# Performance work log

Hardware: AMD Instinct MI355X
Metric: run time of the kernel (lower is better)

The kernel has to match this reference:

```python
import jax, jax.numpy as jnp
import numpy as np

N, E, IN, H, D = 20000, 640000, 256, 4, 32
NEG_SLOPE = 0.2


def setup_inputs() -> dict:
    key = jax.random.key(0)
    ks = jax.random.split(key, 8)
    feat = jax.random.normal(ks[0], (N, IN), dtype=jnp.float32)
    pr_score = jax.random.uniform(ks[1], (N,), dtype=jnp.float32) + 1e-3
    edge_src = jax.random.randint(ks[2], (E,), 0, N)
    edge_dst = jax.random.randint(ks[3], (E,), 0, N)
    # parameters (xavier-ish scale)
    fc_w = jax.random.normal(ks[4], (H * D, IN), dtype=jnp.float32) * (2.0 / np.sqrt(IN + H * D))
    attn_l = jax.random.normal(ks[5], (1, H, D), dtype=jnp.float32) * (2.0 / np.sqrt(1 + D))
    attn_r = jax.random.normal(ks[6], (1, H, D), dtype=jnp.float32) * (2.0 / np.sqrt(1 + D))
    bias = jnp.zeros((H * D,), dtype=jnp.float32)
    return {"feat": feat, "pr_score": pr_score, "edge_src": edge_src,
            "edge_dst": edge_dst, "fc_w": fc_w, "attn_l": attn_l,
            "attn_r": attn_r, "bias": bias}


def reference(feat, pr_score, edge_src, edge_dst, fc_w, attn_l, attn_r, bias):
    n = feat.shape[0]
    h, d = attn_l.shape[1], attn_l.shape[2]
    # feat_src = fc(feat).view(N, H, D)
    ft = (feat @ fc_w.T).reshape(n, h, d)                       # [N,H,D]
    el = jnp.sum(ft * attn_l, axis=-1)                          # [N,H]
    er = jnp.sum(ft * attn_r, axis=-1)                          # [N,H]
    e = jax.nn.leaky_relu(el[edge_src] + er[edge_dst], NEG_SLOPE)  # [E,H]
    # edge_softmax over incoming edges per destination node
    emax = jax.ops.segment_max(e, edge_dst, num_segments=n)
    ee = jnp.exp(e - emax[edge_dst])
    esum = jax.ops.segment_sum(ee, edge_dst, num_segments=n)
    a = ee / esum[edge_dst]                                     # [E,H]
    # PageRank-style normalization: b = pr[src] / sum_{in-edges}(pr[src])
    pr_src = pr_score[edge_src]                                 # [E]
    pr_sum = jax.ops.segment_sum(pr_src, edge_dst, num_segments=n)
    b = pr_src / pr_sum[edge_dst]                               # [E]
    c = a * b[:, None]                                          # [E,H]
    csum = jax.ops.segment_sum(c, edge_dst, num_segments=n)
    c = c / csum[edge_dst]                                      # [E,H]
    # weighted aggregation: rst[dst] = sum_e ft[src_e] * c_e
    m = ft[edge_src] * c[:, :, None]                            # [E,H,D]
    rst = jax.ops.segment_sum(m, edge_dst, num_segments=n)      # [N,H,D]
    rst = rst + bias.reshape(1, h, d)
    return rst
```

## Files before the change

kernel.cpp:

```cpp
#include <hip/hip_runtime.h>

#define IN_DIM 256
#define HD 128
#define NHEAD 4
#define NEG_SLOPE 0.2f
#define ELLW 128

typedef unsigned int  uint;
typedef unsigned short ushort_t;

typedef short bf16x8 __attribute__((ext_vector_type(8)));
typedef float f32x4  __attribute__((ext_vector_type(4)));

__device__ __forceinline__ ushort_t f2bf(float x) {
    uint u = __float_as_uint(x);
    u += 0x7fffu + ((u >> 16) & 1u);
    return (ushort_t)(u >> 16);
}
__device__ __forceinline__ uint pack2(float lo, float hi) {
    return (uint)f2bf(lo) | ((uint)f2bf(hi) << 16);
}
__device__ __forceinline__ float bflo(uint u) { return __uint_as_float(u << 16); }
__device__ __forceinline__ float bfhi(uint u) { return __uint_as_float(u & 0xffff0000u); }

#define GBM 64
#define GBK 64
#define LDK 72

__global__ __launch_bounds__(256) void gemm_mfma(
    const float* __restrict__ feat, const float* __restrict__ fcw,
    const float* __restrict__ attn_l, const float* __restrict__ attn_r,
    ushort_t* __restrict__ ft16, float* __restrict__ el, float* __restrict__ er,
    int* __restrict__ deg, int n)
{
    __shared__ ushort_t s_a[GBM * LDK];
    __shared__ ushort_t s_b[128 * LDK];

    const int t    = threadIdx.x;
    {
        const int z = blockIdx.x * 256 + t;
        if (z < n) deg[z] = 0;
    }

    const int row0 = blockIdx.x * GBM;
    const int w    = t >> 6;
    const int lane = t & 63;
    const int fr   = lane & 15;
    const int fq   = lane >> 4;

    f32x4 acc[8];
#pragma unroll
    for (int nt = 0; nt < 8; ++nt) acc[nt] = (f32x4){0.f, 0.f, 0.f, 0.f};

    const int s_row = t >> 2, s_kca = (t & 3) * 16;
    const int s_col = t >> 1, s_kcb = (t & 1) * 32;

    const ushort_t* pa  = &s_a[(w * 16 + fr) * LDK + fq * 8];
    const ushort_t* pb0 = &s_b[fr * LDK + fq * 8];

    for (int k0 = 0; k0 < IN_DIM; k0 += GBK) {
        {
            const int grow = row0 + s_row;
            float4 v0, v1, v2, v3;
            if (grow < n) {
                const float* p = feat + (size_t)grow * IN_DIM + k0 + s_kca;
                v0 = *(const float4*)(p + 0);
                v1 = *(const float4*)(p + 4);
                v2 = *(const float4*)(p + 8);
                v3 = *(const float4*)(p + 12);
            } else {
                v0 = make_float4(0.f,0.f,0.f,0.f); v1 = v0; v2 = v0; v3 = v0;
            }
            uint4* dst = (uint4*)&s_a[s_row * LDK + s_kca];
            dst[0] = make_uint4(pack2(v0.x,v0.y), pack2(v0.z,v0.w),
                                pack2(v1.x,v1.y), pack2(v1.z,v1.w));
            dst[1] = make_uint4(pack2(v2.x,v2.y), pack2(v2.z,v2.w),
                                pack2(v3.x,v3.y), pack2(v3.z,v3.w));
        }
        {
            const float* p = fcw + (size_t)s_col * IN_DIM + k0 + s_kcb;
            uint4* dst = (uint4*)&s_b[s_col * LDK + s_kcb];
#pragma unroll
            for (int q = 0; q < 2; ++q) {
                float4 u0 = *(const float4*)(p + q * 16 + 0);
                float4 u1 = *(const float4*)(p + q * 16 + 4);
                float4 u2 = *(const float4*)(p + q * 16 + 8);
                float4 u3 = *(const float4*)(p + q * 16 + 12);
                dst[2 * q + 0] = make_uint4(pack2(u0.x,u0.y), pack2(u0.z,u0.w),
                                            pack2(u1.x,u1.y), pack2(u1.z,u1.w));
                dst[2 * q + 1] = make_uint4(pack2(u2.x,u2.y), pack2(u2.z,u2.w),
                                            pack2(u3.x,u3.y), pack2(u3.z,u3.w));
            }
        }
        __syncthreads();

        const bf16x8 a0 = *(const bf16x8*)pa;
        const bf16x8 a1 = *(const bf16x8*)(pa + 32);
#pragma unroll
        for (int nt = 0; nt < 8; ++nt) {
            const ushort_t* pb = pb0 + nt * 16 * LDK;
            const bf16x8 b0 = *(const bf16x8*)pb;
            const bf16x8 b1 = *(const bf16x8*)(pb + 32);
            acc[nt] = __builtin_amdgcn_mfma_f32_16x16x32_bf16(a0, b0, acc[nt], 0, 0, 0);
            acc[nt] = __builtin_amdgcn_mfma_f32_16x16x32_bf16(a1, b1, acc[nt], 0, 0, 0);
        }
        __syncthreads();
    }

    float al[8], ar_[8];
#pragma unroll
    for (int nt = 0; nt < 8; ++nt) {
        al[nt]  = attn_l[nt * 16 + fr];
        ar_[nt] = attn_r[nt * 16 + fr];
    }

#pragma unroll
    for (int j = 0; j < 4; ++j) {
        const int grow = row0 + w * 16 + fq * 4 + j;
        const bool ok = grow < n;
        if (ok) {
#pragma unroll
            for (int nt = 0; nt < 8; ++nt)
                ft16[(size_t)grow * HD + nt * 16 + fr] = f2bf(acc[nt][j]);
        }
        float pl0 = acc[0][j]*al[0] + acc[1][j]*al[1];
        float pl1 = acc[2][j]*al[2] + acc[3][j]*al[3];
        float pl2 = acc[4][j]*al[4] + acc[5][j]*al[5];
        float pl3 = acc[6][j]*al[6] + acc[7][j]*al[7];
        float pe0 = acc[0][j]*ar_[0] + acc[1][j]*ar_[1];
        float pe1 = acc[2][j]*ar_[2] + acc[3][j]*ar_[3];
        float pe2 = acc[4][j]*ar_[4] + acc[5][j]*ar_[5];
        float pe3 = acc[6][j]*ar_[6] + acc[7][j]*ar_[7];
#pragma unroll
        for (int m = 1; m < 16; m <<= 1) {
            pl0 += __shfl_xor(pl0, m, 64); pl1 += __shfl_xor(pl1, m, 64);
            pl2 += __shfl_xor(pl2, m, 64); pl3 += __shfl_xor(pl3, m, 64);
            pe0 += __shfl_xor(pe0, m, 64); pe1 += __shfl_xor(pe1, m, 64);
            pe2 += __shfl_xor(pe2, m, 64); pe3 += __shfl_xor(pe3, m, 64);
        }
        if (ok && fr == 0) {
            *(float4*)&el[(size_t)grow * NHEAD] = make_float4(pl0, pl1, pl2, pl3);
            *(float4*)&er[(size_t)grow * NHEAD] = make_float4(pe0, pe1, pe2, pe3);
        }
    }
}

__global__ void build_ell(const int* __restrict__ src, const int* __restrict__ dst,
                          int* __restrict__ deg, int* __restrict__ ell, int e)
{
    int i = blockIdx.x * blockDim.x + threadIdx.x;
    if (i < e) {
        const int d = dst[i];
        const int r = atomicAdd(&deg[d], 1);
        if (r < ELLW) ell[(size_t)d * ELLW + r] = src[i];
    }
}

__global__ __launch_bounds__(256) void aggregate(
    const uint4* __restrict__ ftu4, const float* __restrict__ el,
    const float* __restrict__ er, const float* __restrict__ pr,
    const int* __restrict__ deg, const int* __restrict__ ell,
    const float* __restrict__ bias, float* __restrict__ out, int n)
{
    const int wave = threadIdx.x >> 6;
    const int lane = threadIdx.x & 63;
    const int slot = lane >> 4;
    const int sub  = lane & 15;
    const int head = sub >> 2;
    const int dst  = blockIdx.x * 4 + wave;

    __shared__ float s_w[4][NHEAD][72];
    __shared__ int   s_s[4][72];

    if (dst >= n) return;

    if (lane < 8) {
        s_s[wave][64 + lane] = 0;
#pragma unroll
        for (int hh = 0; hh < NHEAD; ++hh) s_w[wave][hh][64 + lane] = 0.f;
    }

    const int dg  = min(deg[dst], ELLW);
    const int beg = dst * ELLW;
    const float4 e4 = *(const float4*)&er[(size_t)dst * NHEAD];

    float aA[8], aB[8];
#pragma unroll
    for (int i = 0; i < 8; ++i) { aA[i] = 0.f; aB[i] = 0.f; }
    float w0 = 0.f, w1 = 0.f, w2 = 0.f, w3 = 0.f;

    for (int base = 0; base < dg; base += 64) {
        const int len = min(64, dg - base);
        if (lane < len) {
            const int s = ell[beg + base + lane];
            const float p = pr[s];
            const float4 l4 = *(const float4*)&el[(size_t)s * NHEAD];
            float e0 = l4.x + e4.x, e1 = l4.y + e4.y;
            float e2 = l4.z + e4.z, e3 = l4.w + e4.w;
            e0 = e0 > 0.f ? e0 : NEG_SLOPE * e0;
            e1 = e1 > 0.f ? e1 : NEG_SLOPE * e1;
            e2 = e2 > 0.f ? e2 : NEG_SLOPE * e2;
            e3 = e3 > 0.f ? e3 : NEG_SLOPE * e3;
            const float ww0 = __expf(e0) * p;
            const float ww1 = __expf(e1) * p;
            const float ww2 = __expf(e2) * p;
            const float ww3 = __expf(e3) * p;
            s_w[wave][0][lane] = ww0; s_w[wave][1][lane] = ww1;
            s_w[wave][2][lane] = ww2; s_w[wave][3][lane] = ww3;
            s_s[wave][lane] = s;
            w0 += ww0; w1 += ww1; w2 += ww2; w3 += ww3;
        } else {
            s_w[wave][0][lane] = 0.f; s_w[wave][1][lane] = 0.f;
            s_w[wave][2][lane] = 0.f; s_w[wave][3][lane] = 0.f;
            s_s[wave][lane] = 0;
        }
        for (int j = 0; j < len; j += 8) {
            const int eA = j + slot;
            const int eB = j + 4 + slot;
            const int   sA = s_s[wave][eA];
            const int   sB = s_s[wave][eB];
            const float wA = s_w[wave][head][eA];
            const float wB = s_w[wave][head][eB];
            const uint4 uA = ftu4[(size_t)sA * 16 + sub];
            const uint4 uB = ftu4[(size_t)sB * 16 + sub];
            aA[0] = fmaf(wA, bflo(uA.x), aA[0]);
            aA[1] = fmaf(wA, bfhi(uA.x), aA[1]);
            aA[2] = fmaf(wA, bflo(uA.y), aA[2]);
            aA[3] = fmaf(wA, bfhi(uA.y), aA[3]);
            aA[4] = fmaf(wA, bflo(uA.z), aA[4]);
            aA[5] = fmaf(wA, bfhi(uA.z), aA[5]);
            aA[6] = fmaf(wA, bflo(uA.w), aA[6]);
            aA[7] = fmaf(wA, bfhi(uA.w), aA[7]);
            aB[0] = fmaf(wB, bflo(uB.x), aB[0]);
            aB[1] = fmaf(wB, bfhi(uB.x), aB[1]);
            aB[2] = fmaf(wB, bflo(uB.y), aB[2]);
            aB[3] = fmaf(wB, bfhi(uB.y), aB[3]);
            aB[4] = fmaf(wB, bflo(uB.z), aB[4]);
            aB[5] = fmaf(wB, bfhi(uB.z), aB[5]);
            aB[6] = fmaf(wB, bflo(uB.w), aB[6]);
            aB[7] = fmaf(wB, bfhi(uB.w), aB[7]);
        }
    }

    float a[8];
#pragma unroll
    for (int i = 0; i < 8; ++i) a[i] = aA[i] + aB[i];
#pragma unroll
    for (int i = 0; i < 8; ++i) {
        a[i] += __shfl_xor(a[i], 16, 64);
        a[i] += __shfl_xor(a[i], 32, 64);
    }

#pragma unroll
    for (int m = 1; m < 64; m <<= 1) {
        w0 += __shfl_xor(w0, m, 64);
        w1 += __shfl_xor(w1, m, 64);
        w2 += __shfl_xor(w2, m, 64);
        w3 += __shfl_xor(w3, m, 64);
    }

    if (slot == 0) {
        const float denom = (head == 0) ? w0 : (head == 1) ? w1 : (head == 2) ? w2 : w3;
        const float inv = (dg > 0) ? 1.f / denom : 0.f;
        const float4 b0 = *(const float4*)&bias[8 * sub];
        const float4 b1 = *(const float4*)&bias[8 * sub + 4];
        float4 r0, r1;
        r0.x = a[0] * inv + b0.x; r0.y = a[1] * inv + b0.y;
        r0.z = a[2] * inv + b0.z; r0.w = a[3] * inv + b0.w;
        r1.x = a[4] * inv + b1.x; r1.y = a[5] * inv + b1.y;
        r1.z = a[6] * inv + b1.z; r1.w = a[7] * inv + b1.w;
        *(float4*)&out[(size_t)dst * HD + 8 * sub]     = r0;
        *(float4*)&out[(size_t)dst * HD + 8 * sub + 4] = r1;
    }
}

extern "C" void kernel_launch(void* const* d_in, const int* in_sizes, int n_in,
                              void* d_out, int out_size, void* d_ws, size_t ws_size,
                              hipStream_t stream)
{
    const float* feat   = (const float*)d_in[0];
    const float* pr     = (const float*)d_in[1];
    const int*   esrc   = (const int*)d_in[2];
    const int*   edst   = (const int*)d_in[3];
    const float* fcw    = (const float*)d_in[4];
    const float* attn_l = (const float*)d_in[5];
    const float* attn_r = (const float*)d_in[6];
    const float* bias   = (const float*)d_in[7];
    float* out = (float*)d_out;

    const int n = in_sizes[0] / IN_DIM;
    const int e = in_sizes[2];

    char* ws = (char*)d_ws;
    size_t off = 0;
    auto wsalloc = [&](size_t bytes) -> void* {
        void* p = ws + off;
        off += (bytes + 255) & ~(size_t)255;
        return p;
    };
    ushort_t* ft16 = (ushort_t*)wsalloc((size_t)n * HD * sizeof(ushort_t));
    float* el   = (float*)wsalloc((size_t)n * NHEAD * sizeof(float));
    float* er   = (float*)wsalloc((size_t)n * NHEAD * sizeof(float));
    int*   deg  = (int*)wsalloc((size_t)n * sizeof(int));
    int*   ell  = (int*)wsalloc((size_t)n * ELLW * sizeof(int));

    gemm_mfma<<<(n + GBM - 1) / GBM, 256, 0, stream>>>(feat, fcw, attn_l, attn_r,
                                                       ft16, el, er, deg, n);
    build_ell<<<(e + 255) / 256, 256, 0, stream>>>(esrc, edst, deg, ell, e);
    aggregate<<<(n + 3) / 4, 256, 0, stream>>>((const uint4*)ft16, el, er, pr,
                                               deg, ell, bias, out, n);
}
```

Measured before the change: 81.88 us.

## Fuse GEMM, ELL build and aggregation into one cooperative persistent kernel

```diff
diff --git a/kernel.cpp b/kernel.cpp
--- a/kernel.cpp
+++ b/kernel.cpp
@@ -1,10 +1,18 @@
 #include <hip/hip_runtime.h>
+#include <hip/hip_cooperative_groups.h>
+
+namespace cg = cooperative_groups;
 
 #define IN_DIM 256
 #define HD 128
 #define NHEAD 4
 #define NEG_SLOPE 0.2f
 #define ELLW 128
+#define GBM 64
+#define GBK 64
+#define LDK 72
+#define G_GEMM 320
+#define GRID_F 512
 
 typedef unsigned int  uint;
 typedef unsigned short ushort_t;
@@ -23,26 +31,15 @@
 __device__ __forceinline__ float bflo(uint u) { return __uint_as_float(u << 16); }
 __device__ __forceinline__ float bfhi(uint u) { return __uint_as_float(u & 0xffff0000u); }
 
-#define GBM 64
-#define GBK 64
-#define LDK 72
-
-__global__ __launch_bounds__(256) void gemm_mfma(
+__device__ __forceinline__ void gemm_tile(
+    ushort_t* __restrict__ s_a, ushort_t* __restrict__ s_b, int tile,
     const float* __restrict__ feat, const float* __restrict__ fcw,
     const float* __restrict__ attn_l, const float* __restrict__ attn_r,
     ushort_t* __restrict__ ft16, float* __restrict__ el, float* __restrict__ er,
-    int* __restrict__ deg, int n)
-{
-    __shared__ ushort_t s_a[GBM * LDK];
-    __shared__ ushort_t s_b[128 * LDK];
-
+    int n)
+{
     const int t    = threadIdx.x;
-    {
-        const int z = blockIdx.x * 256 + t;
-        if (z < n) deg[z] = 0;
-    }
-
-    const int row0 = blockIdx.x * GBM;
+    const int row0 = tile * GBM;
     const int w    = t >> 6;
     const int lane = t & 63;
     const int fr   = lane & 15;
@@ -145,40 +142,16 @@
     }
 }
 
-__global__ void build_ell(const int* __restrict__ src, const int* __restrict__ dst,
-                          int* __restrict__ deg, int* __restrict__ ell, int e)
-{
-    int i = blockIdx.x * blockDim.x + threadIdx.x;
-    if (i < e) {
-        const int d = dst[i];
-        const int r = atomicAdd(&deg[d], 1);
-        if (r < ELLW) ell[(size_t)d * ELLW + r] = src[i];
-    }
-}
-
-__global__ __launch_bounds__(256) void aggregate(
+__device__ __forceinline__ void agg_one(
     const uint4* __restrict__ ftu4, const float* __restrict__ el,
     const float* __restrict__ er, const float* __restrict__ pr,
     const int* __restrict__ deg, const int* __restrict__ ell,
-    const float* __restrict__ bias, float* __restrict__ out, int n)
-{
-    const int wave = threadIdx.x >> 6;
-    const int lane = threadIdx.x & 63;
+    const float* __restrict__ bias, float* __restrict__ out,
+    int dst, int lane, float (*__restrict__ sw)[72], int* __restrict__ ss)
+{
     const int slot = lane >> 4;
     const int sub  = lane & 15;
     const int head = sub >> 2;
-    const int dst  = blockIdx.x * 4 + wave;
-
-    __shared__ float s_w[4][NHEAD][72];
-    __shared__ int   s_s[4][72];
-
-    if (dst >= n) return;
-
-    if (lane < 8) {
-        s_s[wave][64 + lane] = 0;
-#pragma unroll
-        for (int hh = 0; hh < NHEAD; ++hh) s_w[wave][hh][64 + lane] = 0.f;
-    }
 
     const int dg  = min(deg[dst], ELLW);
     const int beg = dst * ELLW;
@@ -205,22 +178,22 @@
             const float ww1 = __expf(e1) * p;
             const float ww2 = __expf(e2) * p;
             const float ww3 = __expf(e3) * p;
-            s_w[wave][0][lane] = ww0; s_w[wave][1][lane] = ww1;
-            s_w[wave][2][lane] = ww2; s_w[wave][3][lane] = ww3;
-            s_s[wave][lane] = s;
+            sw[0][lane] = ww0; sw[1][lane] = ww1;
+            sw[2][lane] = ww2; sw[3][lane] = ww3;
+            ss[lane] = s;
             w0 += ww0; w1 += ww1; w2 += ww2; w3 += ww3;
         } else {
-            s_w[wave][0][lane] = 0.f; s_w[wave][1][lane] = 0.f;
-            s_w[wave][2][lane] = 0.f; s_w[wave][3][lane] = 0.f;
-            s_s[wave][lane] = 0;
+            sw[0][lane] = 0.f; sw[1][lane] = 0.f;
+            sw[2][lane] = 0.f; sw[3][lane] = 0.f;
+            ss[lane] = 0;
         }
         for (int j = 0; j < len; j += 8) {
             const int eA = j + slot;
             const int eB = j + 4 + slot;
-            const int   sA = s_s[wave][eA];
-            const int   sB = s_s[wave][eB];
-            const float wA = s_w[wave][head][eA];
-            const float wB = s_w[wave][head][eB];
+            const int   sA = ss[eA];
+            const int   sB = ss[eB];
+            const float wA = sw[head][eA];
+            const float wB = sw[head][eB];
             const uint4 uA = ftu4[(size_t)sA * 16 + sub];
             const uint4 uB = ftu4[(size_t)sB * 16 + sub];
             aA[0] = fmaf(wA, bflo(uA.x), aA[0]);
@@ -274,6 +247,98 @@
     }
 }
 
+__global__ __launch_bounds__(256, 2) void fused_all(
+    const float* __restrict__ feat, const float* __restrict__ pr,
+    const int* __restrict__ esrc, const int* __restrict__ edst,
+    const float* __restrict__ fcw, const float* __restrict__ attn_l,
+    const float* __restrict__ attn_r, const float* __restrict__ bias,
+    float* __restrict__ out, ushort_t* __restrict__ ft16,
+    float* __restrict__ el, float* __restrict__ er,
+    int* __restrict__ deg, int* __restrict__ ell, int n, int e)
+{
+    __shared__ __align__(16) char smem[27648];
+    const int t = threadIdx.x;
+
+    for (int i = blockIdx.x * 256 + t; i < n; i += GRID_F * 256) deg[i] = 0;
+    __threadfence();
+    cg::this_grid().sync();
+
+    if (blockIdx.x < G_GEMM) {
+        ushort_t* s_a = (ushort_t*)smem;
+        ushort_t* s_b = (ushort_t*)(smem + GBM * LDK * 2);
+        for (int tile = blockIdx.x; tile * GBM < n; tile += G_GEMM)
+            gemm_tile(s_a, s_b, tile, feat, fcw, attn_l, attn_r, ft16, el, er, n);
+    } else {
+        for (int i = (blockIdx.x - G_GEMM) * 256 + t; i < e;
+             i += (GRID_F - G_GEMM) * 256) {
+            const int d = edst[i];
+            const int r = atomicAdd(&deg[d], 1);
+            if (r < ELLW) ell[(size_t)d * ELLW + r] = esrc[i];
+        }
+    }
+    __threadfence();
+    cg::this_grid().sync();
+
+    const int wave = t >> 6;
+    const int lane = t & 63;
+    float (*sw)[72] = ((float (*)[72])smem) + wave * NHEAD;
+    int* ss = ((int*)(smem + GRID_F * 0 + 4608)) + wave * 72;
+    if (lane < 8) {
+        ss[64 + lane] = 0;
+#pragma unroll
+        for (int hh = 0; hh < NHEAD; ++hh) sw[hh][64 + lane] = 0.f;
+    }
+    for (int dst = blockIdx.x * 4 + wave; dst < n; dst += GRID_F * 4)
+        agg_one((const uint4*)ft16, el, er, pr, deg, ell, bias, out,
+                dst, lane, sw, ss);
+}
+
+__global__ __launch_bounds__(256) void gemm_mfma_k(
+    const float* __restrict__ feat, const float* __restrict__ fcw,
+    const float* __restrict__ attn_l, const float* __restrict__ attn_r,
+    ushort_t* __restrict__ ft16, float* __restrict__ el, float* __restrict__ er,
+    int* __restrict__ deg, int n)
+{
+    __shared__ __align__(16) char smem[27648];
+    const int z = blockIdx.x * 256 + threadIdx.x;
+    if (z < n) deg[z] = 0;
+    ushort_t* s_a = (ushort_t*)smem;
+    ushort_t* s_b = (ushort_t*)(smem + GBM * LDK * 2);
+    gemm_tile(s_a, s_b, blockIdx.x, feat, fcw, attn_l, attn_r, ft16, el, er, n);
+}
+
+__global__ void build_ell_k(const int* __restrict__ src, const int* __restrict__ dst,
+                            int* __restrict__ deg, int* __restrict__ ell, int e)
+{
+    int i = blockIdx.x * blockDim.x + threadIdx.x;
+    if (i < e) {
+        const int d = dst[i];
+        const int r = atomicAdd(&deg[d], 1);
+        if (r < ELLW) ell[(size_t)d * ELLW + r] = src[i];
+    }
+}
+
+__global__ __launch_bounds__(256) void aggregate_k(
+    const uint4* __restrict__ ftu4, const float* __restrict__ el,
+    const float* __restrict__ er, const float* __restrict__ pr,
+    const int* __restrict__ deg, const int* __restrict__ ell,
+    const float* __restrict__ bias, float* __restrict__ out, int n)
+{
+    __shared__ __align__(16) char smem[5760];
+    const int wave = threadIdx.x >> 6;
+    const int lane = threadIdx.x & 63;
+    float (*sw)[72] = ((float (*)[72])smem) + wave * NHEAD;
+    int* ss = ((int*)(smem + 4608)) + wave * 72;
+    if (lane < 8) {
+        ss[64 + lane] = 0;
+#pragma unroll
+        for (int hh = 0; hh < NHEAD; ++hh) sw[hh][64 + lane] = 0.f;
+    }
+    const int dst = blockIdx.x * 4 + wave;
+    if (dst < n)
+        agg_one(ftu4, el, er, pr, deg, ell, bias, out, dst, lane, sw, ss);
+}
+
 extern "C" void kernel_launch(void* const* d_in, const int* in_sizes, int n_in,
                               void* d_out, int out_size, void* d_ws, size_t ws_size,
                               hipStream_t stream)
@@ -288,8 +353,8 @@
     const float* bias   = (const float*)d_in[7];
     float* out = (float*)d_out;
 
-    const int n = in_sizes[0] / IN_DIM;
-    const int e = in_sizes[2];
+    int n = in_sizes[0] / IN_DIM;
+    int e = in_sizes[2];
 
     char* ws = (char*)d_ws;
     size_t off = 0;
@@ -304,9 +369,16 @@
     int*   deg  = (int*)wsalloc((size_t)n * sizeof(int));
     int*   ell  = (int*)wsalloc((size_t)n * ELLW * sizeof(int));
 
-    gemm_mfma<<<(n + GBM - 1) / GBM, 256, 0, stream>>>(feat, fcw, attn_l, attn_r,
-                                                       ft16, el, er, deg, n);
-    build_ell<<<(e + 255) / 256, 256, 0, stream>>>(esrc, edst, deg, ell, e);
-    aggregate<<<(n + 3) / 4, 256, 0, stream>>>((const uint4*)ft16, el, er, pr,
-                                               deg, ell, bias, out, n);
-}
+    void* args[] = { &feat, &pr, &esrc, &edst, &fcw, &attn_l, &attn_r, &bias,
+                     &out, &ft16, &el, &er, &deg, &ell, &n, &e };
+    hipError_t cerr = hipLaunchCooperativeKernel(fused_all, dim3(GRID_F), dim3(256),
+                                                 args, 0, stream);
+    if (cerr != hipSuccess) {
+        (void)hipGetLastError();
+        gemm_mfma_k<<<(n + GBM - 1) / GBM, 256, 0, stream>>>(
+            feat, fcw, attn_l, attn_r, ft16, el, er, deg, n);
+        build_ell_k<<<(e + 255) / 256, 256, 0, stream>>>(esrc, edst, deg, ell, e);
+        aggregate_k<<<(n + 3) / 4, 256, 0, stream>>>(
+            (const uint4*)ft16, el, er, pr, deg, ell, bias, out, n);
+    }
+}
```

New measurement: 272.3 us. +232.6%, slower.
